# Optimization experiments

Hardware: AMD Instinct MI355X
Metric: run time of the kernel (lower is better)

The kernel has to match this reference:

```python
import jax, jax.numpy as jnp
import numpy as np

NUM_CLASSES = 2   # module init num_classes; class logits have NUM_CLASSES+1 (incl. 'no object')
ORIG_H, ORIG_W = 512, 512  # original input resolution that masks are upsampled to


def setup_inputs() -> dict:
    key = jax.random.key(0)
    k1, k2 = jax.random.split(key)
    B, Q = 8, 100
    h, w = 128, 128  # mask decoder outputs at 1/4 input resolution
    class_queries_logits = jax.random.normal(k1, (B, Q, NUM_CLASSES + 1), dtype=jnp.float32)
    masks_queries_logits = jax.random.normal(k2, (B, Q, h, w), dtype=jnp.float32)
    return {"class_queries_logits": class_queries_logits,
            "masks_queries_logits": masks_queries_logits}


def reference(class_queries_logits, masks_queries_logits):
    B, Q = masks_queries_logits.shape[:2]
    # bilinear upsample to original resolution (align_corners=False == half-pixel centers)
    masks_up = jax.image.resize(masks_queries_logits, (B, Q, ORIG_H, ORIG_W), method="bilinear")
    # softmax over classes (incl. no-object), keep only the first NUM_CLASSES,
    # exactly as the original loop only indexes c in range(num_classes)
    class_probs = jax.nn.softmax(class_queries_logits, axis=-1)[..., :NUM_CLASSES]  # [B,Q,C]
    mask_probs = jax.nn.sigmoid(masks_up)  # [B,Q,H,W]
    # fused replacement for the triple b/q/c Python loop of weighted accumulates
    logits = jnp.einsum("bqc,bqhw->bchw", class_probs, mask_probs)  # [B,C,H,W]
    return logits
```

## Files before the change

kernel.cpp:

```cpp
#include <hip/hip_runtime.h>
#include <math.h>

#define NB 8
#define NQ 100
#define NQH 50
#define NCP1 3
#define NC 2
#define HIN 128
#define WIN 128
#define HOUT 512
#define WOUT 512
#define QSTR (HIN * WIN)
#define QBYTES (QSTR * 4)

#if __has_builtin(__builtin_amdgcn_exp2f)
#define EXP2F(x) __builtin_amdgcn_exp2f(x)
#else
#define EXP2F(x) exp2f(x)
#endif
#if __has_builtin(__builtin_amdgcn_rcpf)
#define RCPF(x) __builtin_amdgcn_rcpf(x)
#else
#define RCPF(x) (1.0f / (x))
#endif

__device__ __forceinline__ float bperm(int byteaddr, float v) {
  return __int_as_float(__builtin_amdgcn_ds_bpermute(byteaddr, __float_as_int(v)));
}

__global__ __launch_bounds__(512, 4)
void m2f_fused(const float* __restrict__ cls,
               const float* __restrict__ masks,
               float* __restrict__ out) {
  const int k   = blockIdx.x;
  const int b   = blockIdx.y;
  const int tid = threadIdx.x;

  __shared__ float2 pq[NQ];
  __shared__ float  part[8][256];

  if (tid < NQ) {
    const float* cl = cls + (b * NQ + tid) * NCP1;
    float a0 = cl[0], a1 = cl[1], a2 = cl[2];
    float mx = fmaxf(a0, fmaxf(a1, a2));
    const float L2E = 1.4426950408889634f;
    float e0 = EXP2F((a0 - mx) * L2E);
    float e1 = EXP2F((a1 - mx) * L2E);
    float e2 = EXP2F((a2 - mx) * L2E);
    float inv = RCPF(e0 + e1 + e2);
    pq[tid] = make_float2(e0 * inv, e1 * inv);
  }
  __syncthreads();

  const int wave = tid >> 6;
  const int r    = wave & 3;
  const int qh   = wave >> 2;
  const int lane = tid & 63;
  const int q0   = qh * NQH;

  const int rlo = (r < 2) ? (k > 0 ? k - 1 : 0) : k;
  const int rhi = (r < 2) ? k : (k < HIN - 1 ? k + 1 : HIN - 1);
  const float NL2E = -1.4426950408889634f;
  const float wlo = ((r == 0) ? 0.375f : (r == 1) ? 0.125f
                   : (r == 2) ? 0.875f : 0.625f) * NL2E;
  const float whi = ((r == 0) ? 0.625f : (r == 1) ? 0.875f
                   : (r == 2) ? 0.125f : 0.375f) * NL2E;

  const int voffA = q0 * QBYTES + (rlo * WIN + 2 * lane) * 4;
  const int voffB = q0 * QBYTES + (rhi * WIN + 2 * lane) * 4;
  const float* const basep = masks + (size_t)b * NQ * QSTR;

  const int addrL = (lane - 1) << 2;
  const int addrR = (lane + 1) << 2;
  const bool edgeL = (lane == 0);
  const bool edgeR = (lane == 63);

  float2 aSL = make_float2(0.f, 0.f);
  float2 aS0 = make_float2(0.f, 0.f);
  float2 aSM = make_float2(0.f, 0.f);
  float2 aS1 = make_float2(0.f, 0.f);

  float2 A0, B0, A1, B1, A2, B2, A3, B3, A4, B4;

#define LOADSET(S, qrel)                                                  \
  do {                                                                    \
    asm volatile("global_load_dwordx2 %0, %2, %3\n\t"                     \
                 "global_load_dwordx2 %1, %4, %3"                         \
                 : "=&v"(A##S), "=&v"(B##S)                               \
                 : "v"(voffA + (qrel) * QBYTES), "s"(basep),              \
                   "v"(voffB + (qrel) * QBYTES));                         \
  } while (0)

#define WAITS(S)                                                          \
  asm volatile("s_waitcnt vmcnt(8)" : "+v"(A##S), "+v"(B##S))

#define COMPUTE(S, qq)                                                    \
  do {                                                                    \
    const float2 pd = pq[qq];                                             \
    float t0 = fmaf(wlo, A##S.x, whi * B##S.x);             \
    float t1 = fmaf(wlo, A##S.y, whi * B##S.y);             \
    float tLr = bperm(addrL, t1);                                         \
    float tL = edgeL ? t0 : tLr;                                          \
    float m01 = 0.5f * (t0 + t1);                                         \
    float mL  = 0.5f * (tL + t0);                                         \
    float s0  = RCPF(1.0f + EXP2F(t0));                                   \
    float s1  = RCPF(1.0f + EXP2F(t1));                                   \
    float sm  = RCPF(1.0f + EXP2F(m01));                                  \
    float sL  = RCPF(1.0f + EXP2F(mL));                                   \
    aSL.x = fmaf(pd.x, sL, aSL.x);  aSL.y = fmaf(pd.y, sL, aSL.y);        \
    aS0.x = fmaf(pd.x, s0, aS0.x);  aS0.y = fmaf(pd.y, s0, aS0.y);        \
    aSM.x = fmaf(pd.x, sm, aSM.x);  aSM.y = fmaf(pd.y, sm, aSM.y);        \
    aS1.x = fmaf(pd.x, s1, aS1.x);  aS1.y = fmaf(pd.y, s1, aS1.y);        \
  } while (0)

  LOADSET(0, 0); LOADSET(1, 1); LOADSET(2, 2); LOADSET(3, 3); LOADSET(4, 4);

  for (int q = 0; q < NQH - 5; q += 5) {
    WAITS(0); COMPUTE(0, q0 + q);     LOADSET(0, q + 5);
    WAITS(1); COMPUTE(1, q0 + q + 1); LOADSET(1, q + 6);
    WAITS(2); COMPUTE(2, q0 + q + 2); LOADSET(2, q + 7);
    WAITS(3); COMPUTE(3, q0 + q + 3); LOADSET(3, q + 8);
    WAITS(4); COMPUTE(4, q0 + q + 4); LOADSET(4, q + 9);
  }

  asm volatile("s_waitcnt vmcnt(0)"
               : "+v"(A0), "+v"(B0), "+v"(A1), "+v"(B1), "+v"(A2), "+v"(B2),
                 "+v"(A3), "+v"(B3), "+v"(A4), "+v"(B4));
  COMPUTE(0, q0 + NQH - 5);
  COMPUTE(1, q0 + NQH - 4);
  COMPUTE(2, q0 + NQH - 3);
  COMPUTE(3, q0 + NQH - 2);
  COMPUTE(4, q0 + NQH - 1);

  const int col = r * 64 + lane;
  if (qh == 1) {
    part[0][col] = aSL.x;  part[1][col] = aSL.y;
    part[2][col] = aS0.x;  part[3][col] = aS0.y;
    part[4][col] = aSM.x;  part[5][col] = aSM.y;
    part[6][col] = aS1.x;  part[7][col] = aS1.y;
  }
  __syncthreads();
  if (qh == 0) {
    aSL.x += part[0][col];  aSL.y += part[1][col];
    aS0.x += part[2][col];  aS0.y += part[3][col];
    aSM.x += part[4][col];  aSM.y += part[5][col];
    aS1.x += part[6][col];  aS1.y += part[7][col];

    float SRx_r = bperm(addrR, aSL.x);
    float SRy_r = bperm(addrR, aSL.y);
    float SRx = edgeR ? aS1.x : SRx_r;
    float SRy = edgeR ? aS1.y : SRy_r;

    float o0x = fmaf(0.25f, aS0.x, 0.75f * aSL.x);
    float o1x = fmaf(0.75f, aS0.x, 0.25f * aSL.x);
    float o2x = fmaf(0.25f, aSM.x, 0.75f * aS0.x);
    float o3x = fmaf(0.75f, aSM.x, 0.25f * aS0.x);
    float o4x = fmaf(0.25f, aS1.x, 0.75f * aSM.x);
    float o5x = fmaf(0.75f, aS1.x, 0.25f * aSM.x);
    float o6x = fmaf(0.25f, SRx,   0.75f * aS1.x);
    float o7x = fmaf(0.75f, SRx,   0.25f * aS1.x);
    float o0y = fmaf(0.25f, aS0.y, 0.75f * aSL.y);
    float o1y = fmaf(0.75f, aS0.y, 0.25f * aSL.y);
    float o2y = fmaf(0.25f, aSM.y, 0.75f * aS0.y);
    float o3y = fmaf(0.75f, aSM.y, 0.25f * aS0.y);
    float o4y = fmaf(0.25f, aS1.y, 0.75f * aSM.y);
    float o5y = fmaf(0.75f, aS1.y, 0.25f * aSM.y);
    float o6y = fmaf(0.25f, SRy,   0.75f * aS1.y);
    float o7y = fmaf(0.75f, SRy,   0.25f * aS1.y);

    const int y  = 4 * k + r;
    const int x0 = 8 * lane;
    float* o0 = out + (((size_t)b * NC + 0) * HOUT + y) * WOUT + x0;
    float* o1 = out + (((size_t)b * NC + 1) * HOUT + y) * WOUT + x0;
    *(float4*)o0       = make_float4(o0x, o1x, o2x, o3x);
    *(float4*)(o0 + 4) = make_float4(o4x, o5x, o6x, o7x);
    *(float4*)o1       = make_float4(o0y, o1y, o2y, o3y);
    *(float4*)(o1 + 4) = make_float4(o4y, o5y, o6y, o7y);
  }
}

extern "C" void kernel_launch(void* const* d_in, const int* in_sizes, int n_in,
                              void* d_out, int out_size, void* d_ws, size_t ws_size,
                              hipStream_t stream) {
  const float* cls   = (const float*)d_in[0];
  const float* masks = (const float*)d_in[1];
  float* out = (float*)d_out;
  dim3 grid(HIN, NB);
  m2f_fused<<<grid, 512, 0, stream>>>(cls, masks, out);
}
```

Before: 111.5 us.

## Replace sigmoid transcendentals with LDS lookup table and linear interpolation

Builds a 2048-entry shared-memory table of sigmoid values and slopes over [-16,16) at each block start. Each sigmoid in the inner loop then becomes a clamp, an index, a fract and an LDS read plus an FMA, replacing exp2 and rcp on the transcendental unit. In exchange it adds LDS traffic with possible bank conflicts, 16KB of extra shared memory per block that may reduce occupancy, per-block table setup, and an approximation error from interpolation and clamping at ±16.

```diff
diff --git a/kernel.cpp b/kernel.cpp
--- a/kernel.cpp
+++ b/kernel.cpp
@@ -23,6 +23,11 @@
 #else
 #define RCPF(x) (1.0f / (x))
 #endif
+#if __has_builtin(__builtin_amdgcn_fractf)
+#define FRACTF(x) __builtin_amdgcn_fractf(x)
+#else
+#define FRACTF(x) ((x) - floorf(x))
+#endif
 
 __device__ __forceinline__ float bperm(int byteaddr, float v) {
   return __int_as_float(__builtin_amdgcn_ds_bpermute(byteaddr, __float_as_int(v)));
@@ -36,8 +41,18 @@
   const int b   = blockIdx.y;
   const int tid = threadIdx.x;
 
+  __shared__ float2 sigtab[2048];
   __shared__ float2 pq[NQ];
   __shared__ float  part[8][256];
+
+#pragma unroll
+  for (int j = 0; j < 4; ++j) {
+    const int i = tid + j * 512;
+    const float x = (float)i * 0.015625f - 16.0f;
+    const float s0 = RCPF(1.0f + EXP2F(x));
+    const float s1 = RCPF(1.0f + EXP2F(x + 0.015625f));
+    sigtab[i] = make_float2(s0, s1 - s0);
+  }
 
   if (tid < NQ) {
     const float* cl = cls + (b * NQ + tid) * NCP1;
@@ -60,11 +75,11 @@
 
   const int rlo = (r < 2) ? (k > 0 ? k - 1 : 0) : k;
   const int rhi = (r < 2) ? k : (k < HIN - 1 ? k + 1 : HIN - 1);
-  const float NL2E = -1.4426950408889634f;
+  const float NL2E64 = -1.4426950408889634f * 64.0f;
   const float wlo = ((r == 0) ? 0.375f : (r == 1) ? 0.125f
-                   : (r == 2) ? 0.875f : 0.625f) * NL2E;
+                   : (r == 2) ? 0.875f : 0.625f) * NL2E64;
   const float whi = ((r == 0) ? 0.625f : (r == 1) ? 0.875f
-                   : (r == 2) ? 0.125f : 0.375f) * NL2E;
+                   : (r == 2) ? 0.125f : 0.375f) * NL2E64;
 
   const int voffA = q0 * QBYTES + (rlo * WIN + 2 * lane) * 4;
   const int voffB = q0 * QBYTES + (rhi * WIN + 2 * lane) * 4;
@@ -94,19 +109,29 @@
 #define WAITS(S)                                                          \
   asm volatile("s_waitcnt vmcnt(8)" : "+v"(A##S), "+v"(B##S))
 
+#define SIG(u, sout)                                                      \
+  do {                                                                    \
+    float uc = fminf(fmaxf((u), 0.0f), 2047.0f);                          \
+    int   ii = (int)uc;                                                   \
+    float fr = FRACTF(uc);                                                \
+    float2 e = sigtab[ii];                                                \
+    sout = fmaf(fr, e.y, e.x);                                            \
+  } while (0)
+
 #define COMPUTE(S, qq)                                                    \
   do {                                                                    \
     const float2 pd = pq[qq];                                             \
-    float t0 = fmaf(wlo, A##S.x, whi * B##S.x);             \
-    float t1 = fmaf(wlo, A##S.y, whi * B##S.y);             \
-    float tLr = bperm(addrL, t1);                                         \
-    float tL = edgeL ? t0 : tLr;                                          \
-    float m01 = 0.5f * (t0 + t1);                                         \
-    float mL  = 0.5f * (tL + t0);                                         \
-    float s0  = RCPF(1.0f + EXP2F(t0));                                   \
-    float s1  = RCPF(1.0f + EXP2F(t1));                                   \
-    float sm  = RCPF(1.0f + EXP2F(m01));                                  \
-    float sL  = RCPF(1.0f + EXP2F(mL));                                   \
+    float u0 = fmaf(wlo, A##S.x, fmaf(whi, B##S.x, 1024.0f));             \
+    float u1 = fmaf(wlo, A##S.y, fmaf(whi, B##S.y, 1024.0f));             \
+    float uLr = bperm(addrL, u1);                                         \
+    float uL = edgeL ? u0 : uLr;                                          \
+    float um  = 0.5f * (u0 + u1);                                         \
+    float umL = 0.5f * (uL + u0);                                         \
+    float sL, s0, sm, s1;                                                 \
+    SIG(umL, sL);                                                         \
+    SIG(u0,  s0);                                                         \
+    SIG(um,  sm);                                                         \
+    SIG(u1,  s1);                                                         \
     aSL.x = fmaf(pd.x, sL, aSL.x);  aSL.y = fmaf(pd.y, sL, aSL.y);        \
     aS0.x = fmaf(pd.x, s0, aS0.x);  aS0.y = fmaf(pd.y, s0, aS0.y);        \
     aSM.x = fmaf(pd.x, sm, aSM.x);  aSM.y = fmaf(pd.y, sm, aSM.y);        \
```

Measured after the change: 113.4 us. Within noise of the previous version (+1.7%).
